# Kernel optimization log

Hardware: AMD Instinct MI355X
Metric: run time of the kernel (lower is better)

## Reference

```python
import jax, jax.numpy as jnp
import numpy as np

N, IN_C, E = 50000, 512, 800000
H, C = 2, 64          # heads, per-head channels
HC = H * C            # 128
OUT_C = 2
B = 64                # number of graphs
EPS = 1e-5
NEG_SLOPE = 0.2


def gat_conv(x, src, dst, W, a_src, a_dst, bias):
    """PyG GATConv (concat=True, add_self_loops already included in src/dst)."""
    n = x.shape[0]
    h = (x @ W).reshape(n, H, C)                      # [N,H,C]
    alpha_src = (h * a_src[None]).sum(-1)             # [N,H]
    alpha_dst = (h * a_dst[None]).sum(-1)             # [N,H]
    e = jax.nn.leaky_relu(alpha_src[src] + alpha_dst[dst], NEG_SLOPE)  # [E,H]
    # segment softmax over incoming edges of each destination node
    m = jax.ops.segment_max(e, dst, num_segments=n)   # [N,H]
    ex = jnp.exp(e - m[dst])
    denom = jax.ops.segment_sum(ex, dst, num_segments=n)
    alpha = ex / denom[dst]                           # [E,H]
    msg = h[src] * alpha[:, :, None]                  # [E,H,C]
    out = jax.ops.segment_sum(msg, dst, num_segments=n)  # [N,H,C]
    return out.reshape(n, HC) + bias


def batch_norm(x, gamma, beta):
    # BatchNorm1d in training mode: batch statistics over the node dim
    mu = x.mean(0)
    var = x.var(0)
    return gamma * (x - mu) * jax.lax.rsqrt(var + EPS) + beta


def setup_inputs() -> dict:
    key = jax.random.key(0)
    ks = jax.random.split(key, 16)
    x = jax.random.normal(ks[0], (N, IN_C), dtype=jnp.float32)
    edge_index = jax.random.randint(ks[1], (2, E), 0, N, dtype=jnp.int64)
    batch = jnp.sort(jax.random.randint(ks[2], (N,), 0, B, dtype=jnp.int64))
    g = lambda k, sh, fan: jax.random.normal(k, sh, dtype=jnp.float32) * (1.0 / np.sqrt(fan))
    return {
        "x": x, "edge_index": edge_index, "batch": batch,
        "W1": g(ks[3], (IN_C, HC), IN_C),
        "att_src1": g(ks[4], (H, C), C), "att_dst1": g(ks[5], (H, C), C),
        "b1": jnp.zeros((HC,), jnp.float32),
        "gamma1": jnp.ones((HC,), jnp.float32), "beta1": jnp.zeros((HC,), jnp.float32),
        "W2": g(ks[6], (HC, HC), HC),
        "att_src2": g(ks[7], (H, C), C), "att_dst2": g(ks[8], (H, C), C),
        "b2": jnp.zeros((HC,), jnp.float32),
        "gamma2": jnp.ones((HC,), jnp.float32), "beta2": jnp.zeros((HC,), jnp.float32),
        "Wlin": g(ks[9], (HC, OUT_C), HC),
        "blin": jnp.zeros((OUT_C,), jnp.float32),
    }


def reference(x, edge_index, batch, W1, att_src1, att_dst1, b1, gamma1, beta1,
              W2, att_src2, att_dst2, b2, gamma2, beta2, Wlin, blin):
    n = x.shape[0]
    # GATConv adds self-loops by default
    loop = jnp.arange(n, dtype=edge_index.dtype)
    src = jnp.concatenate([edge_index[0], loop])
    dst = jnp.concatenate([edge_index[1], loop])

    h = gat_conv(x, src, dst, W1, att_src1, att_dst1, b1)
    h = jax.nn.relu(batch_norm(h, gamma1, beta1))
    h = gat_conv(h, src, dst, W2, att_src2, att_dst2, b2)
    h = jax.nn.relu(batch_norm(h, gamma2, beta2))

    # global mean pool over graphs
    sums = jax.ops.segment_sum(h, batch, num_segments=B)           # [B,HC]
    cnt = jax.ops.segment_sum(jnp.ones((n,), h.dtype), batch, num_segments=B)
    pooled = sums / jnp.maximum(cnt, 1.0)[:, None]
    return pooled @ Wlin + blin                                    # [B,OUT_C]
```

## Files before the change

### kernel.cpp

```cpp
#include <hip/hip_runtime.h>
#include <hip/hip_bf16.h>
#include <cstdint>
#include <cstddef>

#define NN      50000
#define IN_C    512
#define EE      800000
#define ETOT    850000
#define HH      2
#define CC      64
#define HC      128
#define BB      64
#define OUTC    2
#define NEG_SLOPE 0.2f
#define BN_EPS  1e-5f

#define NBLK_SCAN ((NN + 255) / 256)

#define NXCD     8
#define NPX      ((NN + NXCD - 1) / NXCD)
#define EDGES_PER_SLOT 2048
#define NSLOT    ((ETOT + EDGES_PER_SLOT - 1) / EDGES_PER_SLOT)

typedef __bf16 bf16x8 __attribute__((ext_vector_type(8)));
typedef float  f32x4  __attribute__((ext_vector_type(4)));

__device__ __forceinline__ unsigned f2bf(float f) {
    __bf16 b = (__bf16)f;
    return (unsigned)__builtin_bit_cast(unsigned short, b);
}

__device__ __forceinline__ void gload_lds16(const float* g, float* l) {
    __builtin_amdgcn_global_load_lds(
        (const __attribute__((address_space(1))) unsigned*)g,
        (__attribute__((address_space(3))) unsigned*)l,
        16, 0, 0);
}

__global__ __launch_bounds__(256) void deg_kernel(const int* __restrict__ ei, int* __restrict__ deg)
{
    const int xcd  = blockIdx.x & (NXCD - 1);
    const int slot = blockIdx.x >> 3;
    const int lo = xcd * NPX, hi = lo + NPX;
    const int base = slot * EDGES_PER_SLOT;
#pragma unroll
    for (int it = 0; it < EDGES_PER_SLOT / 256; ++it) {
        int e = base + it * 256 + threadIdx.x;
        if (e < ETOT) {
            int d = (e < EE) ? ei[EE + e] : (e - EE);
            if (d >= lo && d < hi) atomicAdd(&deg[d], 1);
        }
    }
}

__global__ __launch_bounds__(256) void bsum_kernel(const int* __restrict__ deg, int* __restrict__ bsum)
{
    int i = blockIdx.x * 256 + threadIdx.x;
    int v = (i < NN) ? deg[i] : 0;
    int lane = threadIdx.x & 63, wv = threadIdx.x >> 6;
#pragma unroll
    for (int o = 32; o > 0; o >>= 1) v += __shfl_down(v, o);
    __shared__ int ws[4];
    if (lane == 0) ws[wv] = v;
    __syncthreads();
    if (threadIdx.x == 0) bsum[blockIdx.x] = ws[0] + ws[1] + ws[2] + ws[3];
}

__global__ __launch_bounds__(256) void bscan_kernel(
    const int* __restrict__ bsum, int* __restrict__ bofs, int* __restrict__ rowp)
{
    int t = threadIdx.x;
    int lane = t & 63, wv = t >> 6;
    int v = (t < NBLK_SCAN) ? bsum[t] : 0;
    int x = v;
#pragma unroll
    for (int o = 1; o < 64; o <<= 1) {
        int y = __shfl_up(x, o);
        if (lane >= o) x += y;
    }
    __shared__ int ws[4];
    if (lane == 63) ws[wv] = x;
    __syncthreads();
    int wo = 0;
#pragma unroll
    for (int w = 0; w < 4; ++w) if (w < wv) wo += ws[w];
    if (t < NBLK_SCAN) bofs[t] = x + wo - v;
    if (t == 0) rowp[NN] = ETOT;
}

__global__ __launch_bounds__(256) void bapply_kernel(
    const int* __restrict__ deg, const int* __restrict__ bofs,
    int* __restrict__ rowp, int* __restrict__ cur)
{
    int i = blockIdx.x * 256 + threadIdx.x;
    int v = (i < NN) ? deg[i] : 0;
    int lane = threadIdx.x & 63, wv = threadIdx.x >> 6;
    int x = v;
#pragma unroll
    for (int o = 1; o < 64; o <<= 1) {
        int y = __shfl_up(x, o);
        if (lane >= o) x += y;
    }
    __shared__ int ws[4];
    if (lane == 63) ws[wv] = x;
    __syncthreads();
    int wo = 0;
#pragma unroll
    for (int w = 0; w < 4; ++w) if (w < wv) wo += ws[w];
    if (i < NN) {
        int r = bofs[blockIdx.x] + x + wo - v;
        rowp[i] = r; cur[i] = r;
    }
}

__global__ __launch_bounds__(256) void scatter_kernel(
    const int* __restrict__ ei, int* __restrict__ cur, int* __restrict__ esrc)
{
    const int xcd  = blockIdx.x & (NXCD - 1);
    const int slot = blockIdx.x >> 3;
    const int lo = xcd * NPX, hi = lo + NPX;
    const int base = slot * EDGES_PER_SLOT;
#pragma unroll
    for (int it = 0; it < EDGES_PER_SLOT / 256; ++it) {
        int e = base + it * 256 + threadIdx.x;
        if (e < ETOT) {
            int s, d;
            if (e < EE) { s = ei[e]; d = ei[EE + e]; }
            else        { s = e - EE; d = s; }
            if (d >= lo && d < hi) {
                int pos = atomicAdd(&cur[d], 1);
                esrc[pos] = s;
            }
        }
    }
}

__global__ __launch_bounds__(256) void wfrag_kernel(
    const float* __restrict__ W, unsigned short* __restrict__ Wf, int K)
{
    int t = blockIdx.x * 256 + threadIdx.x;
    if (t >= K * 16) return;
    int lane = t & 63, frag = t >> 6;
    int kblk = frag >> 3, nt = frag & 7;
    int quad = lane >> 4, ln = lane & 15;
    int kbase = kblk * 32 + quad * 8;
    int n = nt * 16 + ln;
    unsigned short u[8];
#pragma unroll
    for (int j = 0; j < 8; ++j)
        u[j] = (unsigned short)f2bf(W[(size_t)(kbase + j) * HC + n]);
    ushort4 a; a.x = u[0]; a.y = u[1]; a.z = u[2]; a.w = u[3];
    ushort4 b; b.x = u[4]; b.y = u[5]; b.z = u[6]; b.w = u[7];
    *(ushort4*)(Wf + (size_t)t * 8)     = a;
    *(ushort4*)(Wf + (size_t)t * 8 + 4) = b;
}

template<int K, bool AFFINE>
__global__ __launch_bounds__(256) void mfma_gemm_kernel(
    const float* __restrict__ A, const unsigned short* __restrict__ Wf,
    const float* __restrict__ atts, const float* __restrict__ attd,
    unsigned* __restrict__ hb, float* __restrict__ as_, float* __restrict__ ad_,
    const float* __restrict__ sc, const float* __restrict__ sh)
{
    constexpr int NSTEP = K >> 5;
    __shared__ __align__(16) float Abuf[2][64 * 32];

    const int tid  = threadIdx.x;
    const int wave = tid >> 6, lane = tid & 63;
    const int quad = lane >> 4, ln = lane & 15;
    const int m0 = blockIdx.x * 64;

    const int srow = tid >> 3;
    const int g    = (tid & 7) ^ (srow & 7);
    int grow0 = m0 + srow;      if (grow0 > NN - 1) grow0 = NN - 1;
    int grow1 = m0 + srow + 32; if (grow1 > NN - 1) grow1 = NN - 1;
    const float* gsrc0 = A + (size_t)grow0 * K + g * 4;
    const float* gsrc1 = A + (size_t)grow1 * K + g * 4;
    float* ldst0 = &Abuf[0][wave * 256];
    float* ldst1 = &Abuf[0][1024 + wave * 256];
    const int bufstride = 64 * 32;

    const int rr = wave * 16 + ln;
    const int myrow = m0 + rr;
    const int base_f = rr * 32;
    const int sA = (((quad * 2)     ^ (rr & 7)) * 4);
    const int sB = (((quad * 2 + 1) ^ (rr & 7)) * 4);

    const unsigned short* wbase = Wf + lane * 8;

    f32x4 acc[8];
#pragma unroll
    for (int nt = 0; nt < 8; ++nt) acc[nt] = (f32x4){0.f, 0.f, 0.f, 0.f};

    gload_lds16(gsrc0, ldst0);
    gload_lds16(gsrc1, ldst1);
    bf16x8 bfr[2][8];
#pragma unroll
    for (int nt = 0; nt < 8; ++nt) bfr[0][nt] = *(const bf16x8*)(wbase + nt * 512);

#pragma unroll
    for (int ks = 0; ks < NSTEP; ++ks) {
        const int cur = ks & 1;
        __syncthreads();
        if (ks + 1 < NSTEP) {
            gload_lds16(gsrc0 + (size_t)(ks + 1) * 32, ldst0 + (cur ^ 1) * bufstride);
            gload_lds16(gsrc1 + (size_t)(ks + 1) * 32, ldst1 + (cur ^ 1) * bufstride);
        }

        float4 fa = *(const float4*)&Abuf[cur][base_f + sA];
        float4 fb = *(const float4*)&Abuf[cur][base_f + sB];
        float va[8] = {fa.x, fa.y, fa.z, fa.w, fb.x, fb.y, fb.z, fb.w};
        if (AFFINE) {
            const int kk = ks * 32 + quad * 8;
            const float4 s0 = *(const float4*)(sc + kk), s1 = *(const float4*)(sc + kk + 4);
            const float4 h0 = *(const float4*)(sh + kk), h1 = *(const float4*)(sh + kk + 4);
            va[0] = fmaxf(fmaf(s0.x, va[0], h0.x), 0.f);
            va[1] = fmaxf(fmaf(s0.y, va[1], h0.y), 0.f);
            va[2] = fmaxf(fmaf(s0.z, va[2], h0.z), 0.f);
            va[3] = fmaxf(fmaf(s0.w, va[3], h0.w), 0.f);
            va[4] = fmaxf(fmaf(s1.x, va[4], h1.x), 0.f);
            va[5] = fmaxf(fmaf(s1.y, va[5], h1.y), 0.f);
            va[6] = fmaxf(fmaf(s1.z, va[6], h1.z), 0.f);
            va[7] = fmaxf(fmaf(s1.w, va[7], h1.w), 0.f);
        }
        union { bf16x8 v; unsigned short u[8]; } af;
#pragma unroll
        for (int j = 0; j < 8; ++j) af.u[j] = (unsigned short)f2bf(va[j]);

        if (ks + 1 < NSTEP) {
            const unsigned short* wfp = wbase + (size_t)(ks + 1) * 4096;
#pragma unroll
            for (int nt = 0; nt < 8; ++nt)
                bfr[cur ^ 1][nt] = *(const bf16x8*)(wfp + nt * 512);
        }

#pragma unroll
        for (int nt = 0; nt < 8; ++nt)
            acc[nt] = __builtin_amdgcn_mfma_f32_16x16x32_bf16(af.v, bfr[cur][nt], acc[nt], 0, 0, 0);
    }

    float wsv[8], wdv[8];
#pragma unroll
    for (int nt = 0; nt < 8; ++nt) { wsv[nt] = atts[nt * 16 + ln]; wdv[nt] = attd[nt * 16 + ln]; }

    const int mbase = m0 + wave * 16 + quad * 4;
#pragma unroll
    for (int r = 0; r < 4; ++r) {
        int m = mbase + r;
        bool ok = (m < NN);
        float ps0 = 0.f, ps1 = 0.f, pd0 = 0.f, pd1 = 0.f;
#pragma unroll
        for (int nt = 0; nt < 8; ++nt) {
            float v = acc[nt][r];
            if (nt < 4) { ps0 = fmaf(v, wsv[nt], ps0); pd0 = fmaf(v, wdv[nt], pd0); }
            else        { ps1 = fmaf(v, wsv[nt], ps1); pd1 = fmaf(v, wdv[nt], pd1); }
        }
#pragma unroll
        for (int nt = 0; nt < 4; ++nt) {
            unsigned pk = f2bf(acc[nt][r]) | (f2bf(acc[nt + 4][r]) << 16);
            if (ok) hb[(size_t)m * 64 + nt * 16 + ln] = pk;
        }
#pragma unroll
        for (int o = 8; o > 0; o >>= 1) {
            ps0 += __shfl_down(ps0, o); ps1 += __shfl_down(ps1, o);
            pd0 += __shfl_down(pd0, o); pd1 += __shfl_down(pd1, o);
        }
        if (ok && ln == 0) {
            *(float2*)&as_[m * 2] = make_float2(ps0, ps1);
            *(float2*)&ad_[m * 2] = make_float2(pd0, pd1);
        }
    }
}

__global__ __launch_bounds__(256) void gat_agg_kernel(
    const int* __restrict__ rowp, const int* __restrict__ esrc,
    const float* __restrict__ as_, const float* __restrict__ ad_,
    const unsigned* __restrict__ hb, float* __restrict__ out)
{
    int node = (blockIdx.x * 256 + threadIdx.x) >> 6;
    int lane = threadIdx.x & 63;
    if (node >= NN) return;
    int beg = rowp[node], end = rowp[node + 1];
    float2 adv = *(const float2*)&ad_[node * 2];

    float l0 = 0.f, l1 = 0.f, a0 = 0.f, a1 = 0.f;

    for (int j0 = beg; j0 < end; j0 += 64) {
        int nj = min(64, end - j0);
        int   sl  = 0;
        float p0l = 0.f, p1l = 0.f;
        if (j0 + lane < end) {
            sl = esrc[j0 + lane];
            float2 t = *(const float2*)&as_[sl * 2];
            float e0 = t.x + adv.x; e0 = fmaxf(e0, NEG_SLOPE * e0);
            float e1 = t.y + adv.y; e1 = fmaxf(e1, NEG_SLOPE * e1);
            p0l = __expf(e0); p1l = __expf(e1);
        }
        l0 += p0l; l1 += p1l;

        int j = 0;
        for (; j + 4 <= nj; j += 4) {
            int sA = __shfl(sl, j),     sB = __shfl(sl, j + 1);
            int sC = __shfl(sl, j + 2), sD = __shfl(sl, j + 3);
            unsigned uA = hb[(size_t)sA * 64 + lane];
            unsigned uB = hb[(size_t)sB * 64 + lane];
            unsigned uC = hb[(size_t)sC * 64 + lane];
            unsigned uD = hb[(size_t)sD * 64 + lane];
            float pA0 = __shfl(p0l, j),     pA1 = __shfl(p1l, j);
            float pB0 = __shfl(p0l, j + 1), pB1 = __shfl(p1l, j + 1);
            float pC0 = __shfl(p0l, j + 2), pC1 = __shfl(p1l, j + 2);
            float pD0 = __shfl(p0l, j + 3), pD1 = __shfl(p1l, j + 3);
            a0 = fmaf(pA0, __uint_as_float(uA << 16), a0);
            a1 = fmaf(pA1, __uint_as_float(uA & 0xffff0000u), a1);
            a0 = fmaf(pB0, __uint_as_float(uB << 16), a0);
            a1 = fmaf(pB1, __uint_as_float(uB & 0xffff0000u), a1);
            a0 = fmaf(pC0, __uint_as_float(uC << 16), a0);
            a1 = fmaf(pC1, __uint_as_float(uC & 0xffff0000u), a1);
            a0 = fmaf(pD0, __uint_as_float(uD << 16), a0);
            a1 = fmaf(pD1, __uint_as_float(uD & 0xffff0000u), a1);
        }
        for (; j < nj; ++j) {
            int s = __shfl(sl, j);
            unsigned u = hb[(size_t)s * 64 + lane];
            float p0 = __shfl(p0l, j), p1 = __shfl(p1l, j);
            a0 = fmaf(p0, __uint_as_float(u << 16), a0);
            a1 = fmaf(p1, __uint_as_float(u & 0xffff0000u), a1);
        }
    }

#pragma unroll
    for (int o = 1; o < 64; o <<= 1) {
        l0 += __shfl_xor(l0, o); l1 += __shfl_xor(l1, o);
    }
    out[(size_t)node * HC + lane]      = a0 / l0;
    out[(size_t)node * HC + 64 + lane] = a1 / l1;
}

__global__ __launch_bounds__(256) void bn_stats_kernel(
    const float* __restrict__ x, float* __restrict__ stats)
{
    int c = threadIdx.x & 127;
    int half = threadIdx.x >> 7;
    float s = 0.f, sq = 0.f;
    for (int r = blockIdx.x * 2 + half; r < NN; r += gridDim.x * 2) {
        float v = x[(size_t)r * HC + c];
        s += v; sq += v * v;
    }
    __shared__ float ls[256], lq[256];
    ls[threadIdx.x] = s; lq[threadIdx.x] = sq;
    __syncthreads();
    if (half == 0) {
        s += ls[threadIdx.x + 128];
        sq += lq[threadIdx.x + 128];
        atomicAdd(&stats[c], s);
        atomicAdd(&stats[128 + c], sq);
    }
}

__global__ void bn_params_kernel(
    const float* __restrict__ stats, const float* __restrict__ gamma,
    const float* __restrict__ beta, float* __restrict__ sc, float* __restrict__ sh)
{
    int c = threadIdx.x;
    const float inv_n = 1.0f / (float)NN;
    float mu = stats[c] * inv_n;
    float var = stats[128 + c] * inv_n - mu * mu;
    float rs = rsqrtf(var + BN_EPS);
    float s = gamma[c] * rs;
    sc[c] = s;
    sh[c] = beta[c] - mu * s;
}

__global__ __launch_bounds__(256) void pool_kernel(
    const float* __restrict__ x, const float* __restrict__ sc,
    const float* __restrict__ sh, const int* __restrict__ batch,
    float* __restrict__ pool, float* __restrict__ cnt)
{
    int c = threadIdx.x & 127;
    int half = threadIdx.x >> 7;
    int r0 = blockIdx.x * 64;
    int rend = min(r0 + 64, NN);
    float s = sc[c], b = sh[c];
    int cur = -1; float acc = 0.f, ccount = 0.f;
    for (int r = r0 + half; r < rend; r += 2) {
        int g = batch[r];
        if (g != cur) {
            if (cur >= 0) {
                atomicAdd(&pool[cur * HC + c], acc);
                if (c == 0) atomicAdd(&cnt[cur], ccount);
            }
            cur = g; acc = 0.f; ccount = 0.f;
        }
        float v = x[(size_t)r * HC + c];
        acc += fmaxf(fmaf(s, v, b), 0.f);
        ccount += 1.f;
    }
    if (cur >= 0) {
        atomicAdd(&pool[cur * HC + c], acc);
        if (c == 0) atomicAdd(&cnt[cur], ccount);
    }
}

__global__ void final_kernel(
    const float* __restrict__ pool, const float* __restrict__ cnt,
    const float* __restrict__ Wlin, const float* __restrict__ blin,
    float* __restrict__ outp)
{
    int t = threadIdx.x;
    int b = t >> 1, oc = t & 1;
    float inv = 1.f / fmaxf(cnt[b], 1.f);
    float s = blin[oc];
    for (int c = 0; c < HC; ++c)
        s += pool[b * HC + c] * inv * Wlin[c * 2 + oc];
    outp[b * 2 + oc] = s;
}

static constexpr size_t OFF_OUT   = 0;
static constexpr size_t OFF_AS    = OFF_OUT + (size_t)NN*HC;
static constexpr size_t OFF_AD    = OFF_AS  + (size_t)NN*HH;
static constexpr size_t OFF_ST1   = OFF_AD  + (size_t)NN*HH;
static constexpr size_t OFF_ST2   = OFF_ST1 + 256;
static constexpr size_t OFF_SC1   = OFF_ST2 + 256;
static constexpr size_t OFF_SH1   = OFF_SC1 + 128;
static constexpr size_t OFF_SC2   = OFF_SH1 + 128;
static constexpr size_t OFF_SH2   = OFF_SC2 + 128;
static constexpr size_t OFF_POOL  = OFF_SH2 + 128;
static constexpr size_t OFF_CNT   = OFF_POOL+ (size_t)BB*HC;
static constexpr size_t OFF_ZEND  = OFF_CNT + BB;
static constexpr size_t IOFF_DEG  = 0;
static constexpr size_t IOFF_ROWP = IOFF_DEG  + NN;
static constexpr size_t IOFF_CUR  = IOFF_ROWP + NN + 1;
static constexpr size_t IOFF_BSUM = IOFF_CUR  + NN;
static constexpr size_t IOFF_BOFS = IOFF_BSUM + NBLK_SCAN;
static constexpr size_t IOFF_ESRC = IOFF_BOFS + NBLK_SCAN;
static constexpr size_t IOFF_HB   = (IOFF_ESRC + ETOT + 3) & ~(size_t)3;
static constexpr size_t IOFF_WF1  = IOFF_HB + (size_t)NN*64;
static constexpr size_t IOFF_WF2  = IOFF_WF1 + (size_t)IN_C*64;
static constexpr size_t IOFF_END  = IOFF_WF2 + (size_t)HC*64;

extern "C" void kernel_launch(void* const* d_in, const int* in_sizes, int n_in,
                              void* d_out, int out_size, void* d_ws, size_t ws_size,
                              hipStream_t stream)
{
    const float* x       = (const float*)d_in[0];
    const int*   ei      = (const int*)  d_in[1];
    const int*   batch   = (const int*)  d_in[2];
    const float* W1      = (const float*)d_in[3];
    const float* atts1   = (const float*)d_in[4];
    const float* attd1   = (const float*)d_in[5];
    const float* gamma1  = (const float*)d_in[7];
    const float* beta1   = (const float*)d_in[8];
    const float* W2      = (const float*)d_in[9];
    const float* atts2   = (const float*)d_in[10];
    const float* attd2   = (const float*)d_in[11];
    const float* gamma2  = (const float*)d_in[13];
    const float* beta2   = (const float*)d_in[14];
    const float* Wlin    = (const float*)d_in[15];
    const float* blin    = (const float*)d_in[16];
    float* outp = (float*)d_out;

    float* ws    = (float*)d_ws;
    float* out   = ws + OFF_OUT;
    float* as_   = ws + OFF_AS;
    float* ad_   = ws + OFF_AD;
    float* st1   = ws + OFF_ST1;
    float* st2   = ws + OFF_ST2;
    float* sc1   = ws + OFF_SC1;
    float* sh1   = ws + OFF_SH1;
    float* sc2   = ws + OFF_SC2;
    float* sh2   = ws + OFF_SH2;
    float* pool  = ws + OFF_POOL;
    float* cnt   = ws + OFF_CNT;

    int* iws  = (int*)(ws + OFF_ZEND);
    int* deg  = iws + IOFF_DEG;
    int* rowp = iws + IOFF_ROWP;
    int* curp = iws + IOFF_CUR;
    int* bsum = iws + IOFF_BSUM;
    int* bofs = iws + IOFF_BOFS;
    int* esrc = iws + IOFF_ESRC;
    unsigned* hb = (unsigned*)(iws + IOFF_HB);
    unsigned short* Wf1 = (unsigned short*)(iws + IOFF_WF1);
    unsigned short* Wf2 = (unsigned short*)(iws + IOFF_WF2);

    const int BIN_BLK   = NXCD * NSLOT;
    const int GEMM_BLK  = (NN + 63) / 64;
    const int WAVE_BLK  = (NN + 3) / 4;
    const int POOL_BLK  = (NN + 63) / 64;

    hipMemsetAsync(st1, 0, (OFF_ZEND - OFF_ST1) * sizeof(float), stream);
    hipMemsetAsync(deg, 0, NN * sizeof(int), stream);

    wfrag_kernel<<<(IN_C * 16 + 255) / 256, 256, 0, stream>>>(W1, Wf1, IN_C);
    wfrag_kernel<<<(HC   * 16 + 255) / 256, 256, 0, stream>>>(W2, Wf2, HC);
    deg_kernel<<<BIN_BLK, 256, 0, stream>>>(ei, deg);
    bsum_kernel<<<NBLK_SCAN, 256, 0, stream>>>(deg, bsum);
    bscan_kernel<<<1, 256, 0, stream>>>(bsum, bofs, rowp);
    bapply_kernel<<<NBLK_SCAN, 256, 0, stream>>>(deg, bofs, rowp, curp);
    scatter_kernel<<<BIN_BLK, 256, 0, stream>>>(ei, curp, esrc);

    mfma_gemm_kernel<IN_C, false><<<GEMM_BLK, 256, 0, stream>>>(
        x, Wf1, atts1, attd1, hb, as_, ad_, nullptr, nullptr);
    gat_agg_kernel<<<WAVE_BLK, 256, 0, stream>>>(rowp, esrc, as_, ad_, hb, out);
    bn_stats_kernel<<<512, 256, 0, stream>>>(out, st1);
    bn_params_kernel<<<1, 128, 0, stream>>>(st1, gamma1, beta1, sc1, sh1);

    mfma_gemm_kernel<HC, true><<<GEMM_BLK, 256, 0, stream>>>(
        out, Wf2, atts2, attd2, hb, as_, ad_, sc1, sh1);
    gat_agg_kernel<<<WAVE_BLK, 256, 0, stream>>>(rowp, esrc, as_, ad_, hb, out);
    bn_stats_kernel<<<512, 256, 0, stream>>>(out, st2);
    bn_params_kernel<<<1, 128, 0, stream>>>(st2, gamma2, beta2, sc2, sh2);

    pool_kernel<<<POOL_BLK, 256, 0, stream>>>(out, sc2, sh2, batch, pool, cnt);
    final_kernel<<<1, 128, 0, stream>>>(pool, cnt, Wlin, blin, outp);
}
```

Measured before the change: 469.1 us.

## Fuse BN stats into aggregation, deepen GEMM staging, merge weight prep and memsets

Batch-norm statistics are now computed inside the aggregation kernel through a per-block shared-memory reduction and atomics into 64 striped slots, which removes two separate full passes over the output. The GEMM now stages 64 K-columns per barrier instead of 32, halving the number of syncs. The edge gather loop is unrolled to 8 loads to get more loads in flight. The two weight-fragment launches and the two memsets are each merged into one. Costs include more shared memory per GEMM block and a larger stats buffer to zero. The aggregation kernel also drops its node bound guard, which is safe only because NN is a multiple of 4.

New measurement: 418.9 us. 1.12x faster.

```diff
diff --git a/kernel.cpp b/kernel.cpp
--- a/kernel.cpp
+++ b/kernel.cpp
@@ -136,10 +136,17 @@
 }
 
 __global__ __launch_bounds__(256) void wfrag_kernel(
-    const float* __restrict__ W, unsigned short* __restrict__ Wf, int K)
+    const float* __restrict__ W1, unsigned short* __restrict__ Wf1,
+    const float* __restrict__ W2, unsigned short* __restrict__ Wf2)
 {
     int t = blockIdx.x * 256 + threadIdx.x;
-    if (t >= K * 16) return;
+    const float* W; unsigned short* Wf;
+    if (t < IN_C * 16) { W = W1; Wf = Wf1; }
+    else {
+        t -= IN_C * 16;
+        if (t >= HC * 16) return;
+        W = W2; Wf = Wf2;
+    }
     int lane = t & 63, frag = t >> 6;
     int kblk = frag >> 3, nt = frag & 7;
     int quad = lane >> 4, ln = lane & 15;
@@ -163,7 +170,7 @@
     const float* __restrict__ sc, const float* __restrict__ sh)
 {
     constexpr int NSTEP = K >> 5;
-    __shared__ __align__(16) float Abuf[2][64 * 32];
+    __shared__ __align__(16) float Abuf[2][64 * 64];
 
     const int tid  = threadIdx.x;
     const int wave = tid >> 6, lane = tid & 63;
@@ -176,12 +183,8 @@
     int grow1 = m0 + srow + 32; if (grow1 > NN - 1) grow1 = NN - 1;
     const float* gsrc0 = A + (size_t)grow0 * K + g * 4;
     const float* gsrc1 = A + (size_t)grow1 * K + g * 4;
-    float* ldst0 = &Abuf[0][wave * 256];
-    float* ldst1 = &Abuf[0][1024 + wave * 256];
-    const int bufstride = 64 * 32;
 
     const int rr = wave * 16 + ln;
-    const int myrow = m0 + rr;
     const int base_f = rr * 32;
     const int sA = (((quad * 2)     ^ (rr & 7)) * 4);
     const int sB = (((quad * 2 + 1) ^ (rr & 7)) * 4);
@@ -192,23 +195,35 @@
 #pragma unroll
     for (int nt = 0; nt < 8; ++nt) acc[nt] = (f32x4){0.f, 0.f, 0.f, 0.f};
 
-    gload_lds16(gsrc0, ldst0);
-    gload_lds16(gsrc1, ldst1);
+    gload_lds16(gsrc0,      &Abuf[0][wave * 256]);
+    gload_lds16(gsrc1,      &Abuf[0][1024 + wave * 256]);
+    gload_lds16(gsrc0 + 32, &Abuf[0][2048 + wave * 256]);
+    gload_lds16(gsrc1 + 32, &Abuf[0][3072 + wave * 256]);
     bf16x8 bfr[2][8];
 #pragma unroll
     for (int nt = 0; nt < 8; ++nt) bfr[0][nt] = *(const bf16x8*)(wbase + nt * 512);
 
 #pragma unroll
     for (int ks = 0; ks < NSTEP; ++ks) {
-        const int cur = ks & 1;
-        __syncthreads();
-        if (ks + 1 < NSTEP) {
-            gload_lds16(gsrc0 + (size_t)(ks + 1) * 32, ldst0 + (cur ^ 1) * bufstride);
-            gload_lds16(gsrc1 + (size_t)(ks + 1) * 32, ldst1 + (cur ^ 1) * bufstride);
-        }
-
-        float4 fa = *(const float4*)&Abuf[cur][base_f + sA];
-        float4 fb = *(const float4*)&Abuf[cur][base_f + sB];
+        const int sub  = ks & 1;
+        const int cbuf = (ks >> 1) & 1;
+        const int bsel = ks & 1;
+        if (sub == 0) {
+            __syncthreads();
+            if (ks + 2 < NSTEP) {
+                const float* n0 = gsrc0 + (size_t)(ks + 2) * 32;
+                const float* n1 = gsrc1 + (size_t)(ks + 2) * 32;
+                float* db = &Abuf[cbuf ^ 1][wave * 256];
+                gload_lds16(n0,      db);
+                gload_lds16(n1,      db + 1024);
+                gload_lds16(n0 + 32, db + 2048);
+                gload_lds16(n1 + 32, db + 3072);
+            }
+        }
+
+        const float* fb_base = &Abuf[cbuf][sub * 2048 + base_f];
+        float4 fa = *(const float4*)(fb_base + sA);
+        float4 fb = *(const float4*)(fb_base + sB);
         float va[8] = {fa.x, fa.y, fa.z, fa.w, fb.x, fb.y, fb.z, fb.w};
         if (AFFINE) {
             const int kk = ks * 32 + quad * 8;
@@ -231,12 +246,12 @@
             const unsigned short* wfp = wbase + (size_t)(ks + 1) * 4096;
 #pragma unroll
             for (int nt = 0; nt < 8; ++nt)
-                bfr[cur ^ 1][nt] = *(const bf16x8*)(wfp + nt * 512);
+                bfr[bsel ^ 1][nt] = *(const bf16x8*)(wfp + nt * 512);
         }
 
 #pragma unroll
         for (int nt = 0; nt < 8; ++nt)
-            acc[nt] = __builtin_amdgcn_mfma_f32_16x16x32_bf16(af.v, bfr[cur][nt], acc[nt], 0, 0, 0);
+            acc[nt] = __builtin_amdgcn_mfma_f32_16x16x32_bf16(af.v, bfr[bsel][nt], acc[nt], 0, 0, 0);
     }
 
     float wsv[8], wdv[8];
@@ -275,11 +290,13 @@
 __global__ __launch_bounds__(256) void gat_agg_kernel(
     const int* __restrict__ rowp, const int* __restrict__ esrc,
     const float* __restrict__ as_, const float* __restrict__ ad_,
-    const unsigned* __restrict__ hb, float* __restrict__ out)
-{
-    int node = (blockIdx.x * 256 + threadIdx.x) >> 6;
-    int lane = threadIdx.x & 63;
-    if (node >= NN) return;
+    const unsigned* __restrict__ hb, float* __restrict__ out,
+    float* __restrict__ stats)
+{
+    const int tid  = threadIdx.x;
+    const int node = (blockIdx.x * 256 + tid) >> 6;
+    const int wave = tid >> 6;
+    const int lane = tid & 63;
     int beg = rowp[node], end = rowp[node + 1];
     float2 adv = *(const float2*)&ad_[node * 2];
 
@@ -299,32 +316,50 @@
         l0 += p0l; l1 += p1l;
 
         int j = 0;
-        for (; j + 4 <= nj; j += 4) {
-            int sA = __shfl(sl, j),     sB = __shfl(sl, j + 1);
-            int sC = __shfl(sl, j + 2), sD = __shfl(sl, j + 3);
+        for (; j + 8 <= nj; j += 8) {
+            int s0 = __shfl(sl, j),     s1 = __shfl(sl, j + 1);
+            int s2 = __shfl(sl, j + 2), s3 = __shfl(sl, j + 3);
+            int s4 = __shfl(sl, j + 4), s5 = __shfl(sl, j + 5);
+            int s6 = __shfl(sl, j + 6), s7 = __shfl(sl, j + 7);
+            unsigned u0 = hb[(size_t)s0 * 64 + lane];
+            unsigned u1 = hb[(size_t)s1 * 64 + lane];
+            unsigned u2 = hb[(size_t)s2 * 64 + lane];
+            unsigned u3 = hb[(size_t)s3 * 64 + lane];
+            unsigned u4 = hb[(size_t)s4 * 64 + lane];
+            unsigned u5 = hb[(size_t)s5 * 64 + lane];
+            unsigned u6 = hb[(size_t)s6 * 64 + lane];
+            unsigned u7 = hb[(size_t)s7 * 64 + lane];
+            a0 = fmaf(__shfl(p0l, j    ), __uint_as_float(u0 << 16), a0);
+            a1 = fmaf(__shfl(p1l, j    ), __uint_as_float(u0 & 0xffff0000u), a1);
+            a0 = fmaf(__shfl(p0l, j + 1), __uint_as_float(u1 << 16), a0);
+            a1 = fmaf(__shfl(p1l, j + 1), __uint_as_float(u1 & 0xffff0000u), a1);
+            a0 = fmaf(__shfl(p0l, j + 2), __uint_as_float(u2 << 16), a0);
+            a1 = fmaf(__shfl(p1l, j + 2), __uint_as_float(u2 & 0xffff0000u), a1);
+            a0 = fmaf(__shfl(p0l, j + 3), __uint_as_float(u3 << 16), a0);
+            a1 = fmaf(__shfl(p1l, j + 3), __uint_as_float(u3 & 0xffff0000u), a1);
+            a0 = fmaf(__shfl(p0l, j + 4), __uint_as_float(u4 << 16), a0);
+            a1 = fmaf(__shfl(p1l, j + 4), __uint_as_float(u4 & 0xffff0000u), a1);
+            a0 = fmaf(__shfl(p0l, j + 5), __uint_as_float(u5 << 16), a0);
+            a1 = fmaf(__shfl(p1l, j + 5), __uint_as_float(u5 & 0xffff0000u), a1);
+            a0 = fmaf(__shfl(p0l, j + 6), __uint_as_float(u6 << 16), a0);
+            a1 = fmaf(__shfl(p1l, j + 6), __uint_as_float(u6 & 0xffff0000u), a1);
+            a0 = fmaf(__shfl(p0l, j + 7), __uint_as_float(u7 << 16), a0);
+            a1 = fmaf(__shfl(p1l, j + 7), __uint_as_float(u7 & 0xffff0000u), a1);
+        }
+        for (; j + 2 <= nj; j += 2) {
+            int sA = __shfl(sl, j), sB = __shfl(sl, j + 1);
             unsigned uA = hb[(size_t)sA * 64 + lane];
             unsigned uB = hb[(size_t)sB * 64 + lane];
-            unsigned uC = hb[(size_t)sC * 64 + lane];
-            unsigned uD = hb[(size_t)sD * 64 + lane];
-            float pA0 = __shfl(p0l, j),     pA1 = __shfl(p1l, j);
-            float pB0 = __shfl(p0l, j + 1), pB1 = __shfl(p1l, j + 1);
-            float pC0 = __shfl(p0l, j + 2), pC1 = __shfl(p1l, j + 2);
-            float pD0 = __shfl(p0l, j + 3), pD1 = __shfl(p1l, j + 3);
-            a0 = fmaf(pA0, __uint_as_float(uA << 16), a0);
-            a1 = fmaf(pA1, __uint_as_float(uA & 0xffff0000u), a1);
-            a0 = fmaf(pB0, __uint_as_float(uB << 16), a0);
-            a1 = fmaf(pB1, __uint_as_float(uB & 0xffff0000u), a1);
-            a0 = fmaf(pC0, __uint_as_float(uC << 16), a0);
-            a1 = fmaf(pC1, __uint_as_float(uC & 0xffff0000u), a1);
-            a0 = fmaf(pD0, __uint_as_float(uD << 16), a0);
-            a1 = fmaf(pD1, __uint_as_float(uD & 0xffff0000u), a1);
-        }
-        for (; j < nj; ++j) {
+            a0 = fmaf(__shfl(p0l, j    ), __uint_as_float(uA << 16), a0);
+            a1 = fmaf(__shfl(p1l, j    ), __uint_as_float(uA & 0xffff0000u), a1);
+            a0 = fmaf(__shfl(p0l, j + 1), __uint_as_float(uB << 16), a0);
+            a1 = fmaf(__shfl(p1l, j + 1), __uint_as_float(uB & 0xffff0000u), a1);
+        }
+        if (j < nj) {
             int s = __shfl(sl, j);
             unsigned u = hb[(size_t)s * 64 + lane];
-            float p0 = __shfl(p0l, j), p1 = __shfl(p1l, j);
-            a0 = fmaf(p0, __uint_as_float(u << 16), a0);
-            a1 = fmaf(p1, __uint_as_float(u & 0xffff0000u), a1);
+            a0 = fmaf(__shfl(p0l, j), __uint_as_float(u << 16), a0);
+            a1 = fmaf(__shfl(p1l, j), __uint_as_float(u & 0xffff0000u), a1);
         }
     }
 
@@ -332,28 +367,25 @@
     for (int o = 1; o < 64; o <<= 1) {
         l0 += __shfl_xor(l0, o); l1 += __shfl_xor(l1, o);
     }
-    out[(size_t)node * HC + lane]      = a0 / l0;
-    out[(size_t)node * HC + 64 + lane] = a1 / l1;
-}
-
-__global__ __launch_bounds__(256) void bn_stats_kernel(
-    const float* __restrict__ x, float* __restrict__ stats)
-{
-    int c = threadIdx.x & 127;
-    int half = threadIdx.x >> 7;
-    float s = 0.f, sq = 0.f;
-    for (int r = blockIdx.x * 2 + half; r < NN; r += gridDim.x * 2) {
-        float v = x[(size_t)r * HC + c];
-        s += v; sq += v * v;
-    }
-    __shared__ float ls[256], lq[256];
-    ls[threadIdx.x] = s; lq[threadIdx.x] = sq;
+    float v0 = a0 / l0;
+    float v1 = a1 / l1;
+    out[(size_t)node * HC + lane]      = v0;
+    out[(size_t)node * HC + 64 + lane] = v1;
+
+    __shared__ float red[4][256];
+    red[wave][lane]      = v0;
+    red[wave][64 + lane] = v1;
     __syncthreads();
-    if (half == 0) {
-        s += ls[threadIdx.x + 128];
-        sq += lq[threadIdx.x + 128];
-        atomicAdd(&stats[c], s);
-        atomicAdd(&stats[128 + c], sq);
+    if (tid < 128) {
+        float s = 0.f, q = 0.f;
+#pragma unroll
+        for (int w = 0; w < 4; ++w) {
+            float v = red[w][tid];
+            s += v; q = fmaf(v, v, q);
+        }
+        int slot = blockIdx.x & 63;
+        atomicAdd(&stats[slot * 128 + tid], s);
+        atomicAdd(&stats[64 * 128 + slot * 128 + tid], q);
     }
 }
 
@@ -362,9 +394,15 @@
     const float* __restrict__ beta, float* __restrict__ sc, float* __restrict__ sh)
 {
     int c = threadIdx.x;
+    float su = 0.f, sq = 0.f;
+#pragma unroll
+    for (int k = 0; k < 64; ++k) {
+        su += stats[k * 128 + c];
+        sq += stats[64 * 128 + k * 128 + c];
+    }
     const float inv_n = 1.0f / (float)NN;
-    float mu = stats[c] * inv_n;
-    float var = stats[128 + c] * inv_n - mu * mu;
+    float mu = su * inv_n;
+    float var = sq * inv_n - mu * mu;
     float rs = rsqrtf(var + BN_EPS);
     float s = gamma[c] * rs;
     sc[c] = s;
@@ -419,8 +457,8 @@
 static constexpr size_t OFF_AS    = OFF_OUT + (size_t)NN*HC;
 static constexpr size_t OFF_AD    = OFF_AS  + (size_t)NN*HH;
 static constexpr size_t OFF_ST1   = OFF_AD  + (size_t)NN*HH;
-static constexpr size_t OFF_ST2   = OFF_ST1 + 256;
-static constexpr size_t OFF_SC1   = OFF_ST2 + 256;
+static constexpr size_t OFF_ST2   = OFF_ST1 + 2*64*128;
+static constexpr size_t OFF_SC1   = OFF_ST2 + 2*64*128;
 static constexpr size_t OFF_SH1   = OFF_SC1 + 128;
 static constexpr size_t OFF_SC2   = OFF_SH1 + 128;
 static constexpr size_t OFF_SH2   = OFF_SC2 + 128;
@@ -487,12 +525,11 @@
     const int GEMM_BLK  = (NN + 63) / 64;
     const int WAVE_BLK  = (NN + 3) / 4;
     const int POOL_BLK  = (NN + 63) / 64;
-
-    hipMemsetAsync(st1, 0, (OFF_ZEND - OFF_ST1) * sizeof(float), stream);
-    hipMemsetAsync(deg, 0, NN * sizeof(int), stream);
-
-    wfrag_kernel<<<(IN_C * 16 + 255) / 256, 256, 0, stream>>>(W1, Wf1, IN_C);
-    wfrag_kernel<<<(HC   * 16 + 255) / 256, 256, 0, stream>>>(W2, Wf2, HC);
+    const int WFRG_BLK  = (IN_C * 16 + HC * 16 + 255) / 256;
+
+    hipMemsetAsync(st1, 0, (OFF_ZEND - OFF_ST1) * sizeof(float) + NN * sizeof(int), stream);
+
+    wfrag_kernel<<<WFRG_BLK, 256, 0, stream>>>(W1, Wf1, W2, Wf2);
     deg_kernel<<<BIN_BLK, 256, 0, stream>>>(ei, deg);
     bsum_kernel<<<NBLK_SCAN, 256, 0, stream>>>(deg, bsum);
     bscan_kernel<<<1, 256, 0, stream>>>(bsum, bofs, rowp);
@@ -501,14 +538,12 @@
 
     mfma_gemm_kernel<IN_C, false><<<GEMM_BLK, 256, 0, stream>>>(
         x, Wf1, atts1, attd1, hb, as_, ad_, nullptr, nullptr);
-    gat_agg_kernel<<<WAVE_BLK, 256, 0, stream>>>(rowp, esrc, as_, ad_, hb, out);
-    bn_stats_kernel<<<512, 256, 0, stream>>>(out, st1);
+    gat_agg_kernel<<<WAVE_BLK, 256, 0, stream>>>(rowp, esrc, as_, ad_, hb, out, st1);
     bn_params_kernel<<<1, 128, 0, stream>>>(st1, gamma1, beta1, sc1, sh1);
 
     mfma_gemm_kernel<HC, true><<<GEMM_BLK, 256, 0, stream>>>(
         out, Wf2, atts2, attd2, hb, as_, ad_, sc1, sh1);
-    gat_agg_kernel<<<WAVE_BLK, 256, 0, stream>>>(rowp, esrc, as_, ad_, hb, out);
-    bn_stats_kernel<<<512, 256, 0, stream>>>(out, st2);
+    gat_agg_kernel<<<WAVE_BLK, 256, 0, stream>>>(rowp, esrc, as_, ad_, hb, out, st2);
     bn_params_kernel<<<1, 128, 0, stream>>>(st2, gamma2, beta2, sc2, sh2);
 
     pool_kernel<<<POOL_BLK, 256, 0, stream>>>(out, sc2, sh2, batch, pool, cnt);
```
